# Optimization experiments

Measured on AMD Instinct MI355X. Metric: run time of the kernel, lower is better.

## Reference

```python
import jax, jax.numpy as jnp
import numpy as np

B, S, D, H = 128, 1024, 64, 512


def _fo_pool(z, f):
    # z, f: (B, S, H); c_t = f_t * c_{t-1} + (1 - f_t) * z_t
    zT = jnp.swapaxes(z, 0, 1)  # (S, B, H)
    fT = jnp.swapaxes(f, 0, 1)
    c0 = jnp.zeros((z.shape[0], z.shape[2]), dtype=z.dtype)

    def step(c, zf):
        z_t, f_t = zf
        c = f_t * c + (1.0 - f_t) * z_t
        return c, c

    _, cs = jax.lax.scan(step, c0, (zT, fT))
    return jnp.swapaxes(cs, 0, 1)  # (B, S, H)


def _qrnn_layer(x, W, b):
    # window=1 QRNN layer with output gate (fo-pooling)
    g = x @ W + b                      # (B, S, 3H)
    z, f, o = jnp.split(g, 3, axis=-1)
    c = _fo_pool(jnp.tanh(z), jax.nn.sigmoid(f))
    return jax.nn.sigmoid(o) * c


def setup_inputs() -> dict:
    key = jax.random.key(0)
    ks = jax.random.split(key, 7)
    s_in = 1.0 / np.sqrt(D)
    s_h = 1.0 / np.sqrt(H)
    return {
        "x":   jax.random.normal(ks[0], (B, S, D), dtype=jnp.float32),
        "W1":  jax.random.normal(ks[1], (D, 3 * H), dtype=jnp.float32) * s_in,
        "b1":  jnp.zeros((3 * H,), dtype=jnp.float32),
        "W2":  jax.random.normal(ks[2], (H, 3 * H), dtype=jnp.float32) * s_h,
        "b2":  jnp.zeros((3 * H,), dtype=jnp.float32),
        "Wfc": jax.random.normal(ks[3], (H, D), dtype=jnp.float32) * s_h,
        "bfc": jnp.zeros((D,), dtype=jnp.float32),
    }


def reference(x, W1, b1, W2, b2, Wfc, bfc):
    h1 = _qrnn_layer(x, W1, b1)    # (B, S, H); dropout=0.2 is identity at eval
    h2 = _qrnn_layer(h1, W2, b2)   # (B, S, H)
    return h2[:, -1, :] @ Wfc + bfc  # (B, D)
```

## Files before the change

kernel.cpp:

```cpp
#include <hip/hip_runtime.h>


using u16 = unsigned short;
using u32 = unsigned int;

typedef __attribute__((ext_vector_type(8))) short bf16x8;
typedef __attribute__((ext_vector_type(4))) float f32x4;

#define B_  128
#define S_  1024
#define D_  64
#define H_  512
#define N3_ 1536
#define QS_ 256

__device__ __forceinline__ u16 f2bf(float f) {
  u32 u = __builtin_bit_cast(u32, f);
  u = (u + 0x7fffu + ((u >> 16) & 1u)) >> 16;
  return (u16)u;
}
__device__ __forceinline__ float bf2f(u16 h) {
  u32 u = ((u32)h) << 16;
  return __builtin_bit_cast(float, u);
}
__device__ __forceinline__ float sigm(float x) {
  return 1.f / (1.f + __expf(-x));
}
__device__ __forceinline__ float tanh_safe(float x) {
  float ax = fabsf(x);
  float t = __expf(-2.f * ax);
  float r = (1.f - t) / (1.f + t);
  return copysignf(r, x);
}
__device__ __forceinline__ int swz_off(int row, int seg) {
  return row * 64 + (((seg ^ (row & 3) ^ ((row >> 2) & 3)) & 3) << 4);
}

#define WAITV4 asm volatile("s_waitcnt vmcnt(4)" ::: "memory")
#define WAITV0 asm volatile("s_waitcnt vmcnt(0)" ::: "memory")
#define WAITL  asm volatile("s_waitcnt lgkmcnt(0)" ::: "memory")
#define SCHED0 __builtin_amdgcn_sched_barrier(0)
#define SBAR   __builtin_amdgcn_s_barrier()

__global__ __launch_bounds__(256) void prek(const float* __restrict__ W1,
                                            u16* __restrict__ w1t,
                                            const float* __restrict__ W2,
                                            u16* __restrict__ w2t) {
  __shared__ u16 tile[64][65];
  const int bid = blockIdx.x;
  const int t = threadIdx.x;
  const int c = t & 63, r0 = t >> 6;
  if (bid < 24) {
    const int n0 = bid * 64;
#pragma unroll
    for (int i = 0; i < 16; i++) {
      int r = r0 + i * 4;
      tile[r][c] = f2bf(W1[(size_t)r * N3_ + n0 + c]);
    }
    __syncthreads();
#pragma unroll
    for (int i = 0; i < 16; i++) {
      int cc = r0 + i * 4;
      w1t[(size_t)(n0 + cc) * 64 + c] = tile[c][cc];
    }
    return;
  }
  {
    const int j = bid - 24;
    const int n0 = (j % 24) * 64, k0 = (j / 24) * 64;
#pragma unroll
    for (int i = 0; i < 16; i++) {
      int r = r0 + i * 4;
      tile[r][c] = f2bf(W2[(size_t)(k0 + r) * N3_ + n0 + c]);
    }
    __syncthreads();
#pragma unroll
    for (int i = 0; i < 16; i++) {
      int cc = r0 + i * 4;
      w2t[(size_t)(n0 + cc) * H_ + k0 + c] = tile[c][cc];
    }
  }
}

__global__ __launch_bounds__(256) void fused1(const float* __restrict__ x,
                                              const u16* __restrict__ w1t,
                                              const float* __restrict__ b1,
                                              u16* __restrict__ h1q,
                                              float* __restrict__ c1,
                                              int s0, int first) {
  constexpr int T = QS_ / 32;
  __shared__ __align__(16) u16 Aring[2][2048];
  __shared__ u16 zfo[32][392];
  const int t = threadIdx.x;
  const int l = t & 63, wv = t >> 6;
  const int lr = l & 15, lg = l >> 4;
  const int bid = blockIdx.x;
  const int hr = bid >> 7, b = bid & 127;
  const int hb = hr * 128;

  bf16x8 breg[6][2];
  float bias[6];
#pragma unroll
  for (int j = 0; j < 6; j++) {
    int jt = wv * 6 + j;
    int col = (jt < 8) ? (hb + jt * 16)
            : (jt < 16) ? (512 + hb + (jt - 8) * 16)
                        : (1024 + hb + (jt - 16) * 16);
    const u16* wp = w1t + (size_t)(col + lr) * 64 + lg * 8;
    breg[j][0] = *(const bf16x8*)(wp);
    breg[j][1] = *(const bf16x8*)(wp + 32);
    bias[j] = b1[col + lr];
  }

  int srow, ksrc;
  {
    int ktile = t >> 7;
    int w = t & 127;
    int row = w >> 2, pseg = w & 3;
    int lseg = pseg ^ ((row & 3) ^ ((row >> 2) & 3));
    srow = row;
    ksrc = ktile * 32 + lseg * 8;
  }
  const u32 ldsw = (u32)t * 8;

  float c = 0.f;
  const int hmy = wv * 64 + l;
  if (wv < 2 && !first) c = c1[b * 512 + hb + hmy];

  {
    const float* xp = x + ((size_t)b * S_ + s0 + srow) * 64 + ksrc;
    float4 v0 = *(const float4*)(xp);
    float4 v1 = *(const float4*)(xp + 4);
    uint4 xa;
    xa.x = (u32)f2bf(v0.x) | ((u32)f2bf(v0.y) << 16);
    xa.y = (u32)f2bf(v0.z) | ((u32)f2bf(v0.w) << 16);
    xa.z = (u32)f2bf(v1.x) | ((u32)f2bf(v1.y) << 16);
    xa.w = (u32)f2bf(v1.z) | ((u32)f2bf(v1.w) << 16);
    *(uint4*)(&Aring[0][ldsw]) = xa;
  }
  WAITL; SCHED0; SBAR;

  const f32x4 zero4 = {0.f, 0.f, 0.f, 0.f};
  for (int tt = 0; tt < T; ++tt) {
    const int rb = tt & 1;
    SBAR;
    float4 v0, v1;
    const bool more = (tt + 1 < T);
    if (more) {
      const float* xp = x + ((size_t)b * S_ + s0 + (tt + 1) * 32 + srow) * 64 + ksrc;
      v0 = *(const float4*)(xp);
      v1 = *(const float4*)(xp + 4);
    }
    f32x4 acc[2][6];
#pragma unroll
    for (int m = 0; m < 2; m++)
#pragma unroll
      for (int j = 0; j < 6; j++) acc[m][j] = zero4;
    const char* Ab = (const char*)&Aring[rb][0];
#pragma unroll
    for (int kk = 0; kk < 2; kk++) {
      bf16x8 a0 = *(const bf16x8*)(Ab + kk * 2048 + swz_off(lr, lg));
      bf16x8 a1 = *(const bf16x8*)(Ab + kk * 2048 + swz_off(16 + lr, lg));
#pragma unroll
      for (int j = 0; j < 6; j++) {
        acc[0][j] = __builtin_amdgcn_mfma_f32_16x16x32_bf16(a0, breg[j][kk], acc[0][j], 0, 0, 0);
        acc[1][j] = __builtin_amdgcn_mfma_f32_16x16x32_bf16(a1, breg[j][kk], acc[1][j], 0, 0, 0);
      }
    }
#pragma unroll
    for (int j = 0; j < 6; j++) {
      int jt = wv * 6 + j;
      int colL = (jt < 8) ? (jt * 16) : (jt < 16) ? (128 + (jt - 8) * 16)
                                                  : (256 + (jt - 16) * 16);
      const bool isz = (jt < 8);
#pragma unroll
      for (int m = 0; m < 2; m++)
#pragma unroll
        for (int r = 0; r < 4; r++) {
          float g = acc[m][j][r] + bias[j];
          float v = isz ? tanh_safe(g) : sigm(g);
          zfo[m * 16 + lg * 4 + r][colL + lr] = f2bf(v);
        }
    }
    if (more) {
      uint4 xb;
      xb.x = (u32)f2bf(v0.x) | ((u32)f2bf(v0.y) << 16);
      xb.y = (u32)f2bf(v0.z) | ((u32)f2bf(v0.w) << 16);
      xb.z = (u32)f2bf(v1.x) | ((u32)f2bf(v1.y) << 16);
      xb.w = (u32)f2bf(v1.z) | ((u32)f2bf(v1.w) << 16);
      *(uint4*)(&Aring[rb ^ 1][ldsw]) = xb;
    }
    WAITL; SCHED0; SBAR;
    if (wv < 2) {
      u16* hout = h1q + ((size_t)b * QS_ + tt * 32) * 512 + hb + hmy;
#pragma unroll 8
      for (int ss = 0; ss < 32; ss++) {
        float z = bf2f(zfo[ss][hmy]);
        float f = bf2f(zfo[ss][128 + hmy]);
        float o = bf2f(zfo[ss][256 + hmy]);
        c = fmaf(f, c - z, z);
        hout[(size_t)ss * 512] = f2bf(o * c);
      }
    }
  }
  if (wv < 2) c1[b * 512 + hb + hmy] = c;
}

__global__ __launch_bounds__(256) void fused2(const u16* __restrict__ h1q,
                                              const u16* __restrict__ w2t,
                                              const float* __restrict__ b2,
                                              float* __restrict__ c2,
                                              const float* __restrict__ ol,
                                              float* __restrict__ h2l,
                                              int first, int last) {
  constexpr int T = QS_ / 16;
  __shared__ __align__(16) u16 Aring[2][8192];
  __shared__ float zf[16][68];
  const int t = threadIdx.x;
  const int l = t & 63, wv = t >> 6;
  const int lr = l & 15, lg = l >> 4;
  const int bid = blockIdx.x;
  const int hr = bid >> 7, b = bid & 127;

  const int colb = (wv < 2) ? (hr * 32 + wv * 16) : (512 + hr * 32 + (wv - 2) * 16);
  bf16x8 breg[16];
  {
    const u16* wp = w2t + (size_t)(colb + lr) * 512 + lg * 8;
#pragma unroll
    for (int kk = 0; kk < 16; kk++) breg[kk] = *(const bf16x8*)(wp + kk * 32);
  }
  const float bias = b2[colb + lr];

  u32 goff[4];
#pragma unroll
  for (int cc = 0; cc < 4; cc++) {
    int o16 = cc * 256 + t;
    int ktile = o16 >> 6;
    int w = o16 & 63;
    int row = w >> 2, pseg = w & 3;
    int lseg = pseg ^ ((row & 3) ^ ((row >> 2) & 3));
    goff[cc] = (u32)((b * QS_ + row) * 512 + ktile * 32 + lseg * 8);
  }
  float c = 0.f;
  if (wv == 0 && l < 32 && !first) c = c2[b * 512 + hr * 32 + l];

#define STG2(rb, tile) do {                                                    \
    _Pragma("unroll")                                                          \
    for (int cc = 0; cc < 4; cc++)                                             \
      __builtin_amdgcn_global_load_lds(                                        \
        (const __attribute__((address_space(1))) void*)(h1q + goff[cc] + (tile) * 16 * 512), \
        (__attribute__((address_space(3))) void*)(&Aring[rb][cc * 2048 + wv * 512]), 16, 0, 0); \
  } while (0)

  WAITV0;
  STG2(0, 0);

  for (int tt = 0; tt < T; ++tt) {
    const int rb = tt & 1;
    if (tt + 1 < T) { STG2(rb ^ 1, tt + 1); WAITV4; }
    else            { WAITV0; }
    SCHED0; SBAR;

    f32x4 acc = {0.f, 0.f, 0.f, 0.f};
    const char* Ab = (const char*)&Aring[rb][0];
#pragma unroll
    for (int kk = 0; kk < 16; kk++) {
      bf16x8 af = *(const bf16x8*)(Ab + kk * 1024 + swz_off(lr, lg));
      acc = __builtin_amdgcn_mfma_f32_16x16x32_bf16(af, breg[kk], acc, 0, 0, 0);
    }
#pragma unroll
    for (int r = 0; r < 4; r++) {
      float g = acc[r] + bias;
      float v = (wv < 2) ? tanh_safe(g) : sigm(g);
      zf[lg * 4 + r][wv * 16 + lr] = v;
    }
    WAITL; SCHED0; SBAR;
    if (wv == 0 && l < 32) {
#pragma unroll
      for (int ss = 0; ss < 16; ss++) {
        float z = zf[ss][l], f = zf[ss][32 + l];
        c = fmaf(f, c - z, z);
      }
    }
  }
#undef STG2
  if (wv == 0 && l < 32) {
    const int idx = b * 512 + hr * 32 + l;
    c2[idx] = c;
    if (last) h2l[idx] = ol[idx] * c;
  }
}

__global__ __launch_bounds__(256) void o_last_k(const u16* __restrict__ h1q,
                                                const u16* __restrict__ w2t,
                                                const float* __restrict__ b2,
                                                float* __restrict__ olast) {
  __shared__ float hs[H_];
  const int b = blockIdx.x;
  const u16* hrow = h1q + ((size_t)b * QS_ + QS_ - 1) * H_;
  for (int k = threadIdx.x; k < H_; k += 256) hs[k] = bf2f(hrow[k]);
  __syncthreads();
  for (int n = threadIdx.x; n < H_; n += 256) {
    const u16* wr = w2t + (size_t)(1024 + n) * H_;
    float acc = 0.f;
#pragma unroll 8
    for (int k = 0; k < H_; k++) acc = fmaf(hs[k], bf2f(wr[k]), acc);
    olast[(size_t)b * H_ + n] = sigm(acc + b2[1024 + n]);
  }
}

__global__ __launch_bounds__(256) void final_fc(const float* __restrict__ h2l,
                                                const float* __restrict__ Wfc,
                                                const float* __restrict__ bfc,
                                                float* __restrict__ out) {
  __shared__ float red[4][64];
  const int b = blockIdx.x;
  const int t = threadIdx.x, d = t & 63, q = t >> 6;
  const float* hrow = h2l + (size_t)b * H_;
  float acc = 0.f;
#pragma unroll 4
  for (int h = q * 128; h < (q + 1) * 128; h++)
    acc = fmaf(hrow[h], Wfc[(size_t)h * D_ + d], acc);
  red[q][d] = acc;
  __syncthreads();
  if (q == 0)
    out[(size_t)b * D_ + d] = red[0][d] + red[1][d] + red[2][d] + red[3][d] + bfc[d];
}

extern "C" void kernel_launch(void* const* d_in, const int* in_sizes, int n_in,
                              void* d_out, int out_size, void* d_ws, size_t ws_size,
                              hipStream_t stream) {
  (void)in_sizes; (void)n_in; (void)out_size; (void)ws_size;
  const float* x   = (const float*)d_in[0];
  const float* W1  = (const float*)d_in[1];
  const float* b1  = (const float*)d_in[2];
  const float* W2  = (const float*)d_in[3];
  const float* b2  = (const float*)d_in[4];
  const float* Wfc = (const float*)d_in[5];
  const float* bfc = (const float*)d_in[6];
  float* out = (float*)d_out;
  char* ws = (char*)d_ws;

  u16*   h1q   = (u16*)(ws);
  u16*   w2t   = (u16*)(ws + 33554432ull);
  u16*   w1t   = (u16*)(ws + 35127296ull);
  float* c1    = (float*)(ws + 35323904ull);
  float* c2    = (float*)(ws + 35586048ull);
  float* olast = (float*)(ws + 35848192ull);
  float* h2l   = (float*)(ws + 36110336ull);

  prek<<<216, 256, 0, stream>>>(W1, w1t, W2, w2t);
  constexpr int NQ = S_ / QS_;
  for (int q = 0; q < NQ; q++) {
    fused1<<<4 * 128, 256, 0, stream>>>(x, w1t, b1, h1q, c1, q * QS_, q == 0);
    if (q == NQ - 1)
      o_last_k<<<B_, 256, 0, stream>>>(h1q, w2t, b2, olast);
    fused2<<<16 * 128, 256, 0, stream>>>(h1q, w2t, b2, c2, olast, h2l,
                                         q == 0, q == NQ - 1);
  }
  final_fc<<<B_, 256, 0, stream>>>(h2l, Wfc, bfc, out);
}
```

Baseline: 585.4 us.

## Repartition QRNN fused kernels so every wave runs its own scan and pipeline deeper

```diff
diff --git a/kernel.cpp b/kernel.cpp
--- a/kernel.cpp
+++ b/kernel.cpp
@@ -36,6 +36,7 @@
   return row * 64 + (((seg ^ (row & 3) ^ ((row >> 2) & 3)) & 3) << 4);
 }
 
+#define WAITV8 asm volatile("s_waitcnt vmcnt(8)" ::: "memory")
 #define WAITV4 asm volatile("s_waitcnt vmcnt(4)" ::: "memory")
 #define WAITV0 asm volatile("s_waitcnt vmcnt(0)" ::: "memory")
 #define WAITL  asm volatile("s_waitcnt lgkmcnt(0)" ::: "memory")
@@ -82,35 +83,36 @@
   }
 }
 
-__global__ __launch_bounds__(256) void fused1(const float* __restrict__ x,
-                                              const u16* __restrict__ w1t,
-                                              const float* __restrict__ b1,
-                                              u16* __restrict__ h1q,
-                                              float* __restrict__ c1,
-                                              int s0, int first) {
+__global__ __launch_bounds__(256, 2) void fused1(const float* __restrict__ x,
+                                                 const u16* __restrict__ w1t,
+                                                 const float* __restrict__ b1,
+                                                 u16* __restrict__ h1q,
+                                                 float* __restrict__ c1,
+                                                 int s0, int first) {
   constexpr int T = QS_ / 32;
   __shared__ __align__(16) u16 Aring[2][2048];
-  __shared__ u16 zfo[32][392];
+  __shared__ u16 zfb[32 * 132];
+  __shared__ u16 ob[32 * 68];
   const int t = threadIdx.x;
   const int l = t & 63, wv = t >> 6;
   const int lr = l & 15, lg = l >> 4;
   const int bid = blockIdx.x;
   const int hr = bid >> 7, b = bid & 127;
-  const int hb = hr * 128;
-
-  bf16x8 breg[6][2];
-  float bias[6];
-#pragma unroll
-  for (int j = 0; j < 6; j++) {
-    int jt = wv * 6 + j;
-    int col = (jt < 8) ? (hb + jt * 16)
-            : (jt < 16) ? (512 + hb + (jt - 8) * 16)
-                        : (1024 + hb + (jt - 16) * 16);
+  const int hb = hr * 64;
+  const int hw = hb + wv * 16;
+
+  bf16x8 breg[3][2];
+  float bias[3];
+#pragma unroll
+  for (int g = 0; g < 3; g++) {
+    const int col = g * 512 + hw;
     const u16* wp = w1t + (size_t)(col + lr) * 64 + lg * 8;
-    breg[j][0] = *(const bf16x8*)(wp);
-    breg[j][1] = *(const bf16x8*)(wp + 32);
-    bias[j] = b1[col + lr];
-  }
+    breg[g][0] = *(const bf16x8*)(wp);
+    breg[g][1] = *(const bf16x8*)(wp + 32);
+    bias[g] = b1[col + lr];
+  }
+  float c = 0.f;
+  if (l < 16 && !first) c = c1[b * 512 + hw + l];
 
   int srow, ksrc;
   {
@@ -122,10 +124,6 @@
     ksrc = ktile * 32 + lseg * 8;
   }
   const u32 ldsw = (u32)t * 8;
-
-  float c = 0.f;
-  const int hmy = wv * 64 + l;
-  if (wv < 2 && !first) c = c1[b * 512 + hb + hmy];
 
   {
     const float* xp = x + ((size_t)b * S_ + s0 + srow) * 64 + ksrc;
@@ -151,141 +149,165 @@
       v0 = *(const float4*)(xp);
       v1 = *(const float4*)(xp + 4);
     }
-    f32x4 acc[2][6];
+    f32x4 acc[2][3];
 #pragma unroll
     for (int m = 0; m < 2; m++)
 #pragma unroll
-      for (int j = 0; j < 6; j++) acc[m][j] = zero4;
+      for (int g = 0; g < 3; g++) acc[m][g] = zero4;
     const char* Ab = (const char*)&Aring[rb][0];
 #pragma unroll
     for (int kk = 0; kk < 2; kk++) {
       bf16x8 a0 = *(const bf16x8*)(Ab + kk * 2048 + swz_off(lr, lg));
       bf16x8 a1 = *(const bf16x8*)(Ab + kk * 2048 + swz_off(16 + lr, lg));
 #pragma unroll
-      for (int j = 0; j < 6; j++) {
-        acc[0][j] = __builtin_amdgcn_mfma_f32_16x16x32_bf16(a0, breg[j][kk], acc[0][j], 0, 0, 0);
-        acc[1][j] = __builtin_amdgcn_mfma_f32_16x16x32_bf16(a1, breg[j][kk], acc[1][j], 0, 0, 0);
-      }
-    }
-#pragma unroll
-    for (int j = 0; j < 6; j++) {
-      int jt = wv * 6 + j;
-      int colL = (jt < 8) ? (jt * 16) : (jt < 16) ? (128 + (jt - 8) * 16)
-                                                  : (256 + (jt - 16) * 16);
-      const bool isz = (jt < 8);
-#pragma unroll
-      for (int m = 0; m < 2; m++)
-#pragma unroll
-        for (int r = 0; r < 4; r++) {
-          float g = acc[m][j][r] + bias[j];
-          float v = isz ? tanh_safe(g) : sigm(g);
-          zfo[m * 16 + lg * 4 + r][colL + lr] = f2bf(v);
-        }
-    }
+      for (int g = 0; g < 3; g++) {
+        acc[0][g] = __builtin_amdgcn_mfma_f32_16x16x32_bf16(a0, breg[g][kk], acc[0][g], 0, 0, 0);
+        acc[1][g] = __builtin_amdgcn_mfma_f32_16x16x32_bf16(a1, breg[g][kk], acc[1][g], 0, 0, 0);
+      }
+    }
+#pragma unroll
+    for (int m = 0; m < 2; m++)
+#pragma unroll
+      for (int r = 0; r < 4; r++) {
+        const int row = m * 16 + lg * 4 + r;
+        float zv = tanh_safe(acc[m][0][r] + bias[0]);
+        float fv = sigm(acc[m][1][r] + bias[1]);
+        float ov = sigm(acc[m][2][r] + bias[2]);
+        *(u32*)(&zfb[row * 132 + (wv * 16 + lr) * 2]) =
+            (u32)f2bf(zv) | ((u32)f2bf(fv) << 16);
+        ob[row * 68 + wv * 16 + lr] = f2bf(ov);
+      }
     if (more) {
-      uint4 xb;
-      xb.x = (u32)f2bf(v0.x) | ((u32)f2bf(v0.y) << 16);
-      xb.y = (u32)f2bf(v0.z) | ((u32)f2bf(v0.w) << 16);
-      xb.z = (u32)f2bf(v1.x) | ((u32)f2bf(v1.y) << 16);
-      xb.w = (u32)f2bf(v1.z) | ((u32)f2bf(v1.w) << 16);
-      *(uint4*)(&Aring[rb ^ 1][ldsw]) = xb;
+      uint4 xa;
+      xa.x = (u32)f2bf(v0.x) | ((u32)f2bf(v0.y) << 16);
+      xa.y = (u32)f2bf(v0.z) | ((u32)f2bf(v0.w) << 16);
+      xa.z = (u32)f2bf(v1.x) | ((u32)f2bf(v1.y) << 16);
+      xa.w = (u32)f2bf(v1.z) | ((u32)f2bf(v1.w) << 16);
+      *(uint4*)(&Aring[rb ^ 1][ldsw]) = xa;
     }
     WAITL; SCHED0; SBAR;
-    if (wv < 2) {
-      u16* hout = h1q + ((size_t)b * QS_ + tt * 32) * 512 + hb + hmy;
+    if (l < 16) {
+      u16* hout = h1q + ((size_t)b * QS_ + tt * 32) * 512 + hw + l;
+      const u16* zrow = &zfb[(wv * 16 + l) * 2];
+      const u16* orow = &ob[wv * 16 + l];
 #pragma unroll 8
       for (int ss = 0; ss < 32; ss++) {
-        float z = bf2f(zfo[ss][hmy]);
-        float f = bf2f(zfo[ss][128 + hmy]);
-        float o = bf2f(zfo[ss][256 + hmy]);
+        u32 v = *(const u32*)(zrow + ss * 132);
+        float z = bf2f((u16)v), f = bf2f((u16)(v >> 16));
+        float o = bf2f(orow[ss * 68]);
         c = fmaf(f, c - z, z);
         hout[(size_t)ss * 512] = f2bf(o * c);
       }
     }
   }
-  if (wv < 2) c1[b * 512 + hb + hmy] = c;
-}
-
-__global__ __launch_bounds__(256) void fused2(const u16* __restrict__ h1q,
-                                              const u16* __restrict__ w2t,
-                                              const float* __restrict__ b2,
-                                              float* __restrict__ c2,
-                                              const float* __restrict__ ol,
-                                              float* __restrict__ h2l,
-                                              int first, int last) {
+  if (l < 16) c1[b * 512 + hw + l] = c;
+}
+
+__global__ __launch_bounds__(256, 2) void fused2(const u16* __restrict__ h1q,
+                                                 const u16* __restrict__ w2t,
+                                                 const float* __restrict__ b2,
+                                                 float* __restrict__ c2,
+                                                 const float* __restrict__ ol,
+                                                 float* __restrict__ h2l,
+                                                 int first, int last) {
   constexpr int T = QS_ / 16;
-  __shared__ __align__(16) u16 Aring[2][8192];
-  __shared__ float zf[16][68];
+  __shared__ __align__(16) u16 Aring[3][8192];
+  __shared__ u16 zfb[2][16 * 132];
   const int t = threadIdx.x;
   const int l = t & 63, wv = t >> 6;
   const int lr = l & 15, lg = l >> 4;
   const int bid = blockIdx.x;
   const int hr = bid >> 7, b = bid & 127;
-
-  const int colb = (wv < 2) ? (hr * 32 + wv * 16) : (512 + hr * 32 + (wv - 2) * 16);
-  bf16x8 breg[16];
+  const int hb = hr * 64;
+  const int hw = hb + wv * 16;
+
+  bf16x8 bz[16], bff[16];
   {
-    const u16* wp = w2t + (size_t)(colb + lr) * 512 + lg * 8;
-#pragma unroll
-    for (int kk = 0; kk < 16; kk++) breg[kk] = *(const bf16x8*)(wp + kk * 32);
-  }
-  const float bias = b2[colb + lr];
+    const u16* wpz = w2t + (size_t)(hw + lr) * 512 + lg * 8;
+    const u16* wpf = w2t + (size_t)(512 + hw + lr) * 512 + lg * 8;
+#pragma unroll
+    for (int kk = 0; kk < 16; kk++) {
+      bz[kk]  = *(const bf16x8*)(wpz + kk * 32);
+      bff[kk] = *(const bf16x8*)(wpf + kk * 32);
+    }
+  }
+  const float biasz = b2[hw + lr];
+  const float biasf = b2[512 + hw + lr];
+  float c = 0.f;
+  if (l < 16 && !first) c = c2[b * 512 + hw + l];
 
   u32 goff[4];
 #pragma unroll
   for (int cc = 0; cc < 4; cc++) {
-    int o16 = cc * 256 + t;
-    int ktile = o16 >> 6;
-    int w = o16 & 63;
-    int row = w >> 2, pseg = w & 3;
+    int row = l >> 2, pseg = l & 3;
     int lseg = pseg ^ ((row & 3) ^ ((row >> 2) & 3));
+    int ktile = cc * 4 + wv;
     goff[cc] = (u32)((b * QS_ + row) * 512 + ktile * 32 + lseg * 8);
   }
-  float c = 0.f;
-  if (wv == 0 && l < 32 && !first) c = c2[b * 512 + hr * 32 + l];
-
-#define STG2(rb, tile) do {                                                    \
+
+#define STG2(rb_, tile) do {                                                   \
     _Pragma("unroll")                                                          \
     for (int cc = 0; cc < 4; cc++)                                             \
       __builtin_amdgcn_global_load_lds(                                        \
         (const __attribute__((address_space(1))) void*)(h1q + goff[cc] + (tile) * 16 * 512), \
-        (__attribute__((address_space(3))) void*)(&Aring[rb][cc * 2048 + wv * 512]), 16, 0, 0); \
+        (__attribute__((address_space(3))) void*)(&Aring[rb_][cc * 2048 + wv * 512]), 16, 0, 0); \
   } while (0)
 
   WAITV0;
   STG2(0, 0);
-
+  STG2(1, 1);
+
+  const f32x4 zero4 = {0.f, 0.f, 0.f, 0.f};
   for (int tt = 0; tt < T; ++tt) {
-    const int rb = tt & 1;
-    if (tt + 1 < T) { STG2(rb ^ 1, tt + 1); WAITV4; }
-    else            { WAITV0; }
-    SCHED0; SBAR;
-
-    f32x4 acc = {0.f, 0.f, 0.f, 0.f};
+    const int rb = tt % 3;
+    if (tt + 2 < T) { STG2((tt + 2) % 3, tt + 2); WAITV8; }
+    else if (tt + 1 < T) { WAITV4; }
+    else { WAITV0; }
+    WAITL; SCHED0; SBAR; SCHED0;
+
+    f32x4 zl = zero4, zh = zero4, fl = zero4, fh = zero4;
     const char* Ab = (const char*)&Aring[rb][0];
 #pragma unroll
     for (int kk = 0; kk < 16; kk++) {
       bf16x8 af = *(const bf16x8*)(Ab + kk * 1024 + swz_off(lr, lg));
-      acc = __builtin_amdgcn_mfma_f32_16x16x32_bf16(af, breg[kk], acc, 0, 0, 0);
-    }
+      if (kk < 8) {
+        zl = __builtin_amdgcn_mfma_f32_16x16x32_bf16(af, bz[kk],  zl, 0, 0, 0);
+        fl = __builtin_amdgcn_mfma_f32_16x16x32_bf16(af, bff[kk], fl, 0, 0, 0);
+      } else {
+        zh = __builtin_amdgcn_mfma_f32_16x16x32_bf16(af, bz[kk],  zh, 0, 0, 0);
+        fh = __builtin_amdgcn_mfma_f32_16x16x32_bf16(af, bff[kk], fh, 0, 0, 0);
+      }
+    }
+    const int par = tt & 1;
+    f32x4 za = zl + zh, fa = fl + fh;
 #pragma unroll
     for (int r = 0; r < 4; r++) {
-      float g = acc[r] + bias;
-      float v = (wv < 2) ? tanh_safe(g) : sigm(g);
-      zf[lg * 4 + r][wv * 16 + lr] = v;
-    }
-    WAITL; SCHED0; SBAR;
-    if (wv == 0 && l < 32) {
+      float zv = tanh_safe(za[r] + biasz);
+      float fv = sigm(fa[r] + biasf);
+      *(u32*)(&zfb[par][(lg * 4 + r) * 132 + (wv * 16 + lr) * 2]) =
+          (u32)f2bf(zv) | ((u32)f2bf(fv) << 16);
+    }
+    if (tt > 0 && l < 16) {
+      const u16* zrow = &zfb[par ^ 1][(wv * 16 + l) * 2];
 #pragma unroll
       for (int ss = 0; ss < 16; ss++) {
-        float z = zf[ss][l], f = zf[ss][32 + l];
+        u32 v = *(const u32*)(zrow + ss * 132);
+        float z = bf2f((u16)v), f = bf2f((u16)(v >> 16));
         c = fmaf(f, c - z, z);
       }
     }
   }
 #undef STG2
-  if (wv == 0 && l < 32) {
-    const int idx = b * 512 + hr * 32 + l;
+  WAITL; SCHED0; SBAR;
+  if (l < 16) {
+    const u16* zrow = &zfb[(T - 1) & 1][(wv * 16 + l) * 2];
+#pragma unroll
+    for (int ss = 0; ss < 16; ss++) {
+      u32 v = *(const u32*)(zrow + ss * 132);
+      float z = bf2f((u16)v), f = bf2f((u16)(v >> 16));
+      c = fmaf(f, c - z, z);
+    }
+    const int idx = b * 512 + hw + l;
     c2[idx] = c;
     if (last) h2l[idx] = ol[idx] * c;
   }
@@ -352,11 +374,11 @@
   prek<<<216, 256, 0, stream>>>(W1, w1t, W2, w2t);
   constexpr int NQ = S_ / QS_;
   for (int q = 0; q < NQ; q++) {
-    fused1<<<4 * 128, 256, 0, stream>>>(x, w1t, b1, h1q, c1, q * QS_, q == 0);
+    fused1<<<8 * 128, 256, 0, stream>>>(x, w1t, b1, h1q, c1, q * QS_, q == 0);
     if (q == NQ - 1)
       o_last_k<<<B_, 256, 0, stream>>>(h1q, w2t, b2, olast);
-    fused2<<<16 * 128, 256, 0, stream>>>(h1q, w2t, b2, c2, olast, h2l,
-                                         q == 0, q == NQ - 1);
+    fused2<<<8 * 128, 256, 0, stream>>>(h1q, w2t, b2, c2, olast, h2l,
+                                        q == 0, q == NQ - 1);
   }
   final_fc<<<B_, 256, 0, stream>>>(h2l, Wfc, bfc, out);
 }
```

Result: faster. 572.2 us (-2.3%).
